# Performance work log

Hardware: AMD Instinct MI355X
Metric: run time of the kernel (lower is better)

Reference implementation:

```python
import jax, jax.numpy as jnp
import numpy as np
from jax import lax

B, T, C = 8, 1025, 512
HEADS = 8
CACHE = 256          # int(dim * cache_ratio)
CLS = 1
L = 256              # gr_cache memory length
H = W = 32           # sqrt(T - CLS)
EPS = 1e-5


def setup_inputs() -> dict:
    key = jax.random.key(0)
    ks = jax.random.split(key, 40)
    def w(k, shape, scale=0.02):
        return jax.random.normal(k, shape, dtype=jnp.float32) * scale
    inp = {}
    inp['x'] = jax.random.normal(ks[0], (B, T, C), dtype=jnp.float32)
    inp['gr_cache'] = jax.random.normal(ks[1], (1, L, CACHE), dtype=jnp.float32)
    # self-attention (dim=512) params, weights stored (in, out)
    inp['Wq1'] = w(ks[2], (C, C)); inp['bq1'] = jnp.zeros((C,), jnp.float32)
    inp['Wk1'] = w(ks[3], (C, C)); inp['bk1'] = jnp.zeros((C,), jnp.float32)
    inp['Wv1'] = w(ks[4], (C, C)); inp['bv1'] = jnp.zeros((C,), jnp.float32)
    inp['Wo1'] = w(ks[5], (C, C)); inp['bo1'] = jnp.zeros((C,), jnp.float32)
    # memory attention (dim=cache_dim=256) params
    inp['Wq2'] = w(ks[6], (CACHE, CACHE)); inp['bq2'] = jnp.zeros((CACHE,), jnp.float32)
    inp['Wk2'] = w(ks[7], (CACHE, CACHE)); inp['bk2'] = jnp.zeros((CACHE,), jnp.float32)
    inp['Wv2'] = w(ks[8], (CACHE, CACHE)); inp['bv2'] = jnp.zeros((CACHE,), jnp.float32)
    inp['Wo2'] = w(ks[9], (CACHE, CACHE)); inp['bo2'] = jnp.zeros((CACHE,), jnp.float32)
    # GRU-style gate linears: in = 2*cache_dim, out = cache_dim
    inp['Wr'] = w(ks[10], (2 * CACHE, CACHE)); inp['br'] = jnp.zeros((CACHE,), jnp.float32)
    inp['Wz'] = w(ks[11], (2 * CACHE, CACHE)); inp['bz'] = jnp.zeros((CACHE,), jnp.float32)
    inp['Wa'] = w(ks[12], (2 * CACHE, CACHE)); inp['ba'] = jnp.zeros((CACHE,), jnp.float32)
    # LayerNorm(cache_dim)
    inp['gamma'] = jnp.ones((CACHE,), jnp.float32)
    inp['beta'] = jnp.zeros((CACHE,), jnp.float32)
    # per-head gate logits, init to -1 as in the module
    inp['lam'] = jnp.full((HEADS,), -1.0, dtype=jnp.float32)
    # grouped conv pos-emb: Conv2d(512, 512, k=3, groups=CACHE) -> (O=512, I/g=2, 3, 3)
    inp['conv_w'] = w(ks[13], (C, C // CACHE, 3, 3))
    inp['conv_b'] = jnp.zeros((C,), jnp.float32)
    return inp


def _mha(q_in, kv_in, Wq, bq, Wk, bk, Wv, bv, Wo, bo):
    Bq, Tq, D = q_in.shape
    Tk = kv_in.shape[1]
    dh = D // HEADS
    q = (q_in @ Wq + bq).reshape(Bq, Tq, HEADS, dh)
    k = (kv_in @ Wk + bk).reshape(Bq, Tk, HEADS, dh)
    v = (kv_in @ Wv + bv).reshape(Bq, Tk, HEADS, dh)
    s = jnp.einsum('bqhd,bkhd->bhqk', q, k) * (1.0 / np.sqrt(dh)).astype(np.float32)
    a = jax.nn.softmax(s, axis=-1)
    o = jnp.einsum('bhqk,bkhd->bqhd', a, v).reshape(Bq, Tq, D)
    return o @ Wo + bo


def reference(x, gr_cache, Wq1, bq1, Wk1, bk1, Wv1, bv1, Wo1, bo1,
              Wq2, bq2, Wk2, bk2, Wv2, bv2, Wo2, bo2,
              Wr, br, Wz, bz, Wa, ba, gamma, beta, lam, conv_w, conv_b):
    B_, T_, C_ = x.shape
    # ---- spatial positional embedding (faithful to torch view->permute quirk) ----
    tok = x[:, CLS:, :].reshape(B_, H, W, C_).transpose(0, 3, 1, 2)   # (B, C, H, W)
    pos = lax.conv_general_dilated(tok, conv_w, (1, 1), 'SAME',
                                   feature_group_count=CACHE,
                                   dimension_numbers=('NCHW', 'OIHW', 'NCHW'))
    pos = pos + conv_b[None, :, None, None]
    pos = pos.reshape(B_, C_, T_ - CLS).transpose(0, 2, 1)            # (B, T-1, C)
    pos = jnp.concatenate([jnp.zeros((B_, CLS, C_), pos.dtype), pos], axis=1)
    # ---- self attention ----
    x_self = _mha(x, x, Wq1, bq1, Wk1, bk1, Wv1, bv1, Wo1, bo1)       # (B, T, C)
    x_self_h = x_self.reshape(B_, T_, HEADS, C_ // HEADS)
    # ---- GRU-style gated cache update ----
    gr = jnp.broadcast_to(gr_cache, (B_, L, CACHE))
    x_summary = x_self[:, :, :CACHE]
    idx = (jnp.arange(L) * T_) // L                                   # nearest interpolate T -> L
    x_summary = x_summary[:, idx, :]                                  # (B, L, CACHE)
    cat = jnp.concatenate([gr, x_summary], axis=-1)
    reset = jax.nn.sigmoid(cat @ Wr + br)
    z = jax.nn.sigmoid(cat @ Wz + bz)
    cat2 = jnp.concatenate([reset * gr, x_summary], axis=-1)
    add = jax.nn.gelu(cat2 @ Wa + ba, approximate=False)
    mu = add.mean(-1, keepdims=True)
    var = ((add - mu) ** 2).mean(-1, keepdims=True)
    add = (add - mu) / jnp.sqrt(var + EPS) * gamma + beta             # LayerNorm
    gr_new = z * add + (1.0 - z) * gr
    # ---- memory attention on first cache_dim channels ----
    x_mem = _mha(x[:, :, :CACHE], gr_new, Wq2, bq2, Wk2, bk2, Wv2, bv2, Wo2, bo2)
    x_mem = x_mem.reshape(B_, T_, HEADS, CACHE // HEADS)
    # ---- per-head alpha blend with zero-padded mem branch ----
    alpha = jax.nn.sigmoid(lam).reshape(1, 1, HEADS, 1)
    pad = jnp.zeros((B_, T_, HEADS, (C_ - CACHE) // HEADS), x.dtype)
    out = (alpha * jnp.concatenate([x_mem, pad], axis=-1)
           + (1.0 - alpha) * x_self_h).reshape(B_, T_, C_) + pos
    return out
```

## Files before the change

kernel.cpp:

```cpp
#include <hip/hip_runtime.h>
#include <math.h>

typedef unsigned short u16;
typedef unsigned int u32;
typedef __attribute__((ext_vector_type(8))) short short8;
typedef __attribute__((ext_vector_type(4))) short short4v;
typedef __attribute__((ext_vector_type(4))) float f32x4;

constexpr int Bc = 8;
constexpr int Tt = 1025;
constexpr int Cc = 512;
constexpr int Hn = 8;
constexpr int CA = 256;
constexpr int Ll = 256;

#if __has_builtin(__builtin_amdgcn_exp2f)
#define EXP2F __builtin_amdgcn_exp2f
#else
#define EXP2F exp2f
#endif

__device__ __forceinline__ u16 f2bf(float f) {
  u32 u = __builtin_bit_cast(u32, f);
  u = (u + 0x7FFFu + ((u >> 16) & 1u)) >> 16;
  return (u16)u;
}
__device__ __forceinline__ u32 pack2f(float lo, float hi) {
  const u32 a = __builtin_bit_cast(u32, hi) + 0x8000u;
  const u32 b = __builtin_bit_cast(u32, lo) + 0x8000u;
  return __builtin_amdgcn_perm(a, b, 0x07060302u);
}

struct WC { const float* s; u16* d; int sN; int sK; int kshift; int tot; };
struct WCP { WC w[11]; };

__global__ void wcast_k(WCP p) {
  const WC a = p.w[blockIdx.y];
  const int kmask = (1 << a.kshift) - 1;
  for (int idx = blockIdx.x * 256 + threadIdx.x; idx < a.tot; idx += gridDim.x * 256) {
    const int k = idx & kmask;
    const int n = idx >> a.kshift;
    a.d[idx] = (k < a.sK) ? f2bf(a.s[(size_t)k * a.sN + n]) : (u16)0;
  }
}

enum { EP_NONE = 0, EP_SIGMOID = 1, EP_GELU = 2 };

struct GemmEpi {
  const float* bias[4];
  int start[4];
  float scale[4];
  int nreg;
};

template <int AF32, int OUTBF, int ACT>
__global__ __launch_bounds__(256) void gemm_mfma(
    const void* __restrict__ Av, int lda,
    const u16* __restrict__ Wt,
    GemmEpi epi,
    void* __restrict__ Cout,
    int M, int N, int K)
{
  __shared__ u16 As[128][32];
  __shared__ u16 Bs[128][32];
  const int tid = threadIdx.x;
  const int m0 = blockIdx.y * 128, n0 = blockIdx.x * 128;
  const int ln = tid & 15, quad = (tid >> 4) & 3, wv = tid >> 6;
  const int wm = (wv & 1) * 64, wn = (wv >> 1) * 64;
  const int sr = tid >> 1;
  const int sk = (tid & 1) * 16;

  f32x4 zf = {0.f, 0.f, 0.f, 0.f};
  f32x4 acc[4][4];
  #pragma unroll
  for (int i = 0; i < 4; i++)
    #pragma unroll
    for (int j = 0; j < 4; j++) acc[i][j] = zf;

  const short8 z8 = {0, 0, 0, 0, 0, 0, 0, 0};

  for (int k0 = 0; k0 < K; k0 += 32) {
    const int gm = m0 + sr;
    short8 a0 = z8, a1 = z8;
    if (gm < M) {
      if (AF32) {
        const float* p = (const float*)Av + (size_t)gm * lda + k0 + sk;
        const float4 f0 = *(const float4*)(p + 0);
        const float4 f1 = *(const float4*)(p + 4);
        const float4 f2 = *(const float4*)(p + 8);
        const float4 f3 = *(const float4*)(p + 12);
        ((u32*)&a0)[0] = pack2f(f0.x, f0.y);
        ((u32*)&a0)[1] = pack2f(f0.z, f0.w);
        ((u32*)&a0)[2] = pack2f(f1.x, f1.y);
        ((u32*)&a0)[3] = pack2f(f1.z, f1.w);
        ((u32*)&a1)[0] = pack2f(f2.x, f2.y);
        ((u32*)&a1)[1] = pack2f(f2.z, f2.w);
        ((u32*)&a1)[2] = pack2f(f3.x, f3.y);
        ((u32*)&a1)[3] = pack2f(f3.z, f3.w);
      } else {
        const u16* p = (const u16*)Av + (size_t)gm * lda + k0 + sk;
        a0 = *(const short8*)p;
        a1 = *(const short8*)(p + 8);
      }
    }
    *(short8*)&As[sr][sk] = a0;
    *(short8*)&As[sr][sk + 8] = a1;
    {
      const u16* q = Wt + (size_t)(n0 + sr) * K + k0 + sk;
      *(short8*)&Bs[sr][sk] = *(const short8*)q;
      *(short8*)&Bs[sr][sk + 8] = *(const short8*)(q + 8);
    }
    __syncthreads();

    short8 af[4], bf[4];
    #pragma unroll
    for (int i = 0; i < 4; i++) af[i] = *(const short8*)&As[wm + i * 16 + ln][quad * 8];
    #pragma unroll
    for (int j = 0; j < 4; j++) bf[j] = *(const short8*)&Bs[wn + j * 16 + ln][quad * 8];
    #pragma unroll
    for (int i = 0; i < 4; i++)
      #pragma unroll
      for (int j = 0; j < 4; j++)
        acc[i][j] = __builtin_amdgcn_mfma_f32_16x16x32_bf16(af[i], bf[j], acc[i][j], 0, 0, 0);
    __syncthreads();
  }

  int ri = 0;
  #pragma unroll
  for (int i = 1; i < 4; i++)
    if (i < epi.nreg && epi.start[i] <= n0) ri = i;
  const float* bp = epi.bias[ri] - epi.start[ri];
  const float sc = epi.scale[ri];

  float bj[4];
  #pragma unroll
  for (int j = 0; j < 4; j++) bj[j] = bp[n0 + wn + j * 16 + ln];

  #pragma unroll
  for (int i = 0; i < 4; i++) {
    #pragma unroll
    for (int r = 0; r < 4; r++) {
      const int gm = m0 + wm + i * 16 + quad * 4 + r;
      if (gm >= M) continue;
      #pragma unroll
      for (int j = 0; j < 4; j++) {
        float v = (acc[i][j][r] + bj[j]) * sc;
        if (ACT == EP_SIGMOID)   v = 1.f / (1.f + __expf(-v));
        else if (ACT == EP_GELU) v = 0.5f * v * (1.f + erff(v * 0.70710678118654752f));
        const size_t off = (size_t)gm * N + n0 + wn + j * 16 + ln;
        if (OUTBF) ((u16*)Cout)[off] = f2bf(v);
        else       ((float*)Cout)[off] = v;
      }
    }
  }
}

template <int DH>
__global__ __launch_bounds__(256) void attn_mfma(
    const u16* __restrict__ Qp, const u16* __restrict__ Kp,
    const u16* __restrict__ Vp, u16* __restrict__ Op,
    int Tq, int Tk, int qbs, int kbs, int obs, int qrs, int krs, int ors)
{
  constexpr int NC = DH / 32;
  constexpr int NM = DH / 16;
  constexpr int VTE = 2 * DH * 32;
  constexpr int PAY = 2 * NM * 4 + 2;
  constexpr int PSTR = PAY | 1;

  __shared__ __align__(16) char smem[2 * VTE * 2 + 4 * 1024 * 2];
  static_assert(128 * PSTR * 4 <= 2 * VTE * 2 + 4 * 1024 * 2, "combine fits");
  u16* const VtP = (u16*)smem;
  u16* const PbP = (u16*)(smem + 2 * VTE * 2);

  const int b = blockIdx.y >> 3, h = blockIdx.y & 7;
  const int q0 = blockIdx.x * 64;
  const int tid = threadIdx.x;
  const int wv = tid >> 6;
  const int pair = wv >> 1;
  const int wvp = wv & 1;
  const int lane = tid & 63;
  const int ln = lane & 15, quad = lane >> 4;
  const int lt = tid & 127;

  const u16* Qb = Qp + (size_t)b * qbs + h * DH;
  const u16* Kb = Kp + (size_t)b * kbs + h * DH;
  const u16* Vb = Vp + (size_t)b * kbs + h * DH;
  u16* Ob = Op + (size_t)b * obs + h * DH;

  const short8 z8 = {0, 0, 0, 0, 0, 0, 0, 0};
  const f32x4 zf = {0.f, 0.f, 0.f, 0.f};

  short8 qf[2][NC];
  #pragma unroll
  for (int qs = 0; qs < 2; qs++) {
    const int gq = q0 + wvp * 32 + qs * 16 + ln;
    #pragma unroll
    for (int c = 0; c < NC; c++) {
      if (gq < Tq) qf[qs][c] = *(const short8*)(Qb + (size_t)gq * qrs + c * 32 + quad * 8);
      else         qf[qs][c] = z8;
    }
  }

  f32x4 oacc[2][NM];
  float lsum[2] = {0.f, 0.f};
  #pragma unroll
  for (int qs = 0; qs < 2; qs++)
    #pragma unroll
    for (int c = 0; c < NM; c++) oacc[qs][c] = zf;

  const int vd0 = (lt & 15) * (DH / 16);
  const int vk = (lt >> 4) * 4;
  const int gb = vk >> 3, off = vk & 7;

  const int nfull = Tk >> 5;
  const int nit = (Tk + 31) >> 5;
  const int tkm1 = Tk - 1;
  const int np = (nit + 1) >> 1;
  const int it0 = pair * np;
  const int itE = it0 + np;

  auto loadK = [&](int it, short8 (&kf)[2][NC]) {
    #pragma unroll
    for (int kc = 0; kc < 2; kc++)
      #pragma unroll
      for (int c = 0; c < NC; c++) {
        int row = (it << 5) + kc * 16 + ln;
        row = row < tkm1 ? row : tkm1;
        kf[kc][c] = *(const short8*)(Kb + (size_t)row * krs + c * 32 + quad * 8);
      }
  };
  auto loadV = [&](int it, short4v (&vr)[4]) {
    #pragma unroll
    for (int i2 = 0; i2 < 4; i2++) {
      int gk = (it << 5) + vk + i2;
      gk = gk < tkm1 ? gk : tkm1;
      short4v t = {0, 0, 0, 0};
      if (DH == 64) {
        t = *(const short4v*)(Vb + (size_t)gk * krs + vd0);
      } else {
        ushort2 u = *(const ushort2*)(Vb + (size_t)gk * krs + vd0);
        t[0] = (short)u.x; t[1] = (short)u.y;
      }
      vr[i2] = t;
    }
  };

  auto body = [&](int it, short8 (&kfC)[2][NC], short4v (&vrC)[4],
                  short8 (&kfN)[2][NC], short4v (&vrN)[4]) {
    const bool full = (it < nfull);
    u16* vt = VtP + pair * VTE + (it & 1) * (DH * 32);
    const int k0 = it << 5;

    #pragma unroll
    for (int i = 0; i < DH / 16; i++) {
      const int d = vd0 + i;
      const int h2 = (d ^ (d >> 3)) & 3;
      short4v w = {vrC[0][i], vrC[1][i], vrC[2][i], vrC[3][i]};
      *(short4v*)&vt[d * 32 + ((gb ^ h2) << 3) + off] = w;
    }
    if (it + 1 < itE) { loadK(it + 1, kfN); loadV(it + 1, vrN); }
    __syncthreads();

    #pragma unroll
    for (int qs = 0; qs < 2; qs++) {
      #pragma unroll
      for (int kc = 0; kc < 2; kc++) {
        f32x4 s = zf;
        #pragma unroll
        for (int c = 0; c < NC; c++)
          s = __builtin_amdgcn_mfma_f32_16x16x32_bf16(kfC[kc][c], qf[qs][c], s, 0, 0, 0);
        float p0, p1, p2, p3;
        if (full) {
          p0 = EXP2F(s[0]); p1 = EXP2F(s[1]); p2 = EXP2F(s[2]); p3 = EXP2F(s[3]);
        } else {
          const int kb = k0 + kc * 16 + quad * 4;
          p0 = (kb + 0 < Tk) ? EXP2F(s[0]) : 0.f;
          p1 = (kb + 1 < Tk) ? EXP2F(s[1]) : 0.f;
          p2 = (kb + 2 < Tk) ? EXP2F(s[2]) : 0.f;
          p3 = (kb + 3 < Tk) ? EXP2F(s[3]) : 0.f;
        }
        lsum[qs] += (p0 + p1) + (p2 + p3);
        short4v pw;
        ((u32*)&pw)[0] = pack2f(p0, p1);
        ((u32*)&pw)[1] = pack2f(p2, p3);
        const int q = qs * 16 + ln;
        const int g = ((kc * 2 + (quad >> 1)) ^ (ln & 3)) & 3;
        *(short4v*)&PbP[wv * 1024 + q * 32 + (g << 3) + (quad & 1) * 4] = pw;
      }
    }

    short8 pf2[2];
    #pragma unroll
    for (int qs = 0; qs < 2; qs++) {
      const int q = qs * 16 + ln;
      const int g = quad ^ (ln & 3);
      pf2[qs] = *(const short8*)&PbP[wv * 1024 + q * 32 + g * 8];
    }
    #pragma unroll
    for (int c = 0; c < NM; c++) {
      const int d = c * 16 + ln;
      const int g = quad ^ ((d ^ (d >> 3)) & 3);
      const short8 vf = *(const short8*)&vt[d * 32 + g * 8];
      #pragma unroll
      for (int qs = 0; qs < 2; qs++)
        oacc[qs][c] = __builtin_amdgcn_mfma_f32_16x16x32_bf16(pf2[qs], vf, oacc[qs][c], 0, 0, 0);
    }
  };

  short8 kfA[2][NC], kfB[2][NC];
  short4v vrA[4], vrB[4];
  loadK(it0, kfA);
  loadV(it0, vrA);

  int j = 0;
  for (; j + 1 < np; j += 2) {
    body(it0 + j, kfA, vrA, kfB, vrB);
    body(it0 + j + 1, kfB, vrB, kfA, vrA);
  }
  if (j < np) body(it0 + j, kfA, vrA, kfB, vrB);

  __syncthreads();
  float* const cbuf = (float*)smem;
  if (wv >= 2) {
    float* dst = cbuf + ((wv - 2) * 64 + lane) * PSTR;
    int idx = 0;
    #pragma unroll
    for (int qs = 0; qs < 2; qs++)
      #pragma unroll
      for (int c = 0; c < NM; c++)
        #pragma unroll
        for (int r = 0; r < 4; r++) dst[idx++] = oacc[qs][c][r];
    dst[idx++] = lsum[0];
    dst[idx]   = lsum[1];
  }
  __syncthreads();
  if (wv >= 2) return;
  {
    const float* src = cbuf + (wv * 64 + lane) * PSTR;
    int idx = 0;
    #pragma unroll
    for (int qs = 0; qs < 2; qs++)
      #pragma unroll
      for (int c = 0; c < NM; c++)
        #pragma unroll
        for (int r = 0; r < 4; r++) oacc[qs][c][r] += src[idx++];
    lsum[0] += src[idx++];
    lsum[1] += src[idx];
  }

  float lq[2];
  #pragma unroll
  for (int qs = 0; qs < 2; qs++) {
    float t = lsum[qs];
    t += __shfl_xor(t, 16);
    t += __shfl_xor(t, 32);
    lq[qs] = t;
  }
  #pragma unroll
  for (int qs = 0; qs < 2; qs++) {
    #pragma unroll
    for (int r = 0; r < 4; r++) {
      const float linv = 1.f / __shfl(lq[qs], quad * 4 + r);
      const int gq = q0 + wvp * 32 + qs * 16 + quad * 4 + r;
      if (gq >= Tq) continue;
      #pragma unroll
      for (int c = 0; c < NM; c++)
        Ob[(size_t)gq * ors + c * 16 + ln] = f2bf(oacc[qs][c][r] * linv);
    }
  }
}

__global__ __launch_bounds__(256) void conv_combine(
    const float* __restrict__ x, const float* __restrict__ cw,
    const float* __restrict__ cb, const float* __restrict__ x_self,
    const float* __restrict__ x_mem, const float* __restrict__ lam,
    float* __restrict__ out)
{
  const int bh = blockIdx.x;
  const int b = bh >> 5, hh = bh & 31;
  const int c = (blockIdx.y << 8) + threadIdx.x;
  const int ci = c & ~1;
  const int dd = c & 63;
  const int h8 = c >> 6;
  const float alpha = 1.f / (1.f + __expf(-lam[h8]));
  const float bias = cb[c];

  float wgt[2][9];
  #pragma unroll
  for (int ch = 0; ch < 2; ch++)
    #pragma unroll
    for (int k = 0; k < 9; k++) wgt[ch][k] = cw[c * 18 + ch * 9 + k];

  const float* xrow[3];
  bool rv[3];
  #pragma unroll
  for (int r = 0; r < 3; r++) {
    const int h2 = hh + r - 1;
    rv[r] = (unsigned)h2 < 32u;
    xrow[r] = x + ((size_t)(b * Tt) + 1 + h2 * 32) * Cc + ci;
  }

  float2 win[3][3];
  #pragma unroll
  for (int r = 0; r < 3; r++) {
    win[r][0] = make_float2(0.f, 0.f);
    win[r][1] = rv[r] ? *(const float2*)(xrow[r]) : make_float2(0.f, 0.f);
  }

  const size_t bT = (size_t)b * Tt;
  for (int w = 0; w < 32; w++) {
    #pragma unroll
    for (int r = 0; r < 3; r++)
      win[r][2] = (rv[r] && w + 1 < 32) ? *(const float2*)(xrow[r] + (w + 1) * Cc)
                                        : make_float2(0.f, 0.f);
    float pos = bias;
    #pragma unroll
    for (int r = 0; r < 3; r++)
      #pragma unroll
      for (int col = 0; col < 3; col++) {
        pos += win[r][col].x * wgt[0][r * 3 + col];
        pos += win[r][col].y * wgt[1][r * 3 + col];
      }
    const size_t bt = bT + 1 + hh * 32 + w;
    const float mem = (dd < 32) ? x_mem[bt * 256 + h8 * 32 + dd] : 0.f;
    out[bt * 512 + c] = pos + alpha * mem + (1.f - alpha) * x_self[bt * 512 + c];
    #pragma unroll
    for (int r = 0; r < 3; r++) { win[r][0] = win[r][1]; win[r][1] = win[r][2]; }
  }

  if (hh == 0) {
    const float mem = (dd < 32) ? x_mem[bT * 256 + h8 * 32 + dd] : 0.f;
    out[bT * 512 + c] = alpha * mem + (1.f - alpha) * x_self[bT * 512 + c];
  }
}

__global__ void build_cat(const float* __restrict__ gr_cache,
                          const float* __restrict__ x_self,
                          u16* __restrict__ cat)
{
  const int idx = blockIdx.x * 256 + threadIdx.x;
  if (idx >= Bc * Ll * 512) return;
  const int k = idx & 511;
  const int bi = idx >> 9;
  const int i = bi & 255;
  const int b = bi >> 8;
  float v;
  if (k < 256) v = gr_cache[i * 256 + k];
  else         v = x_self[((size_t)(b * Tt + 4 * i)) * Cc + (k - 256)];
  cat[idx] = f2bf(v);
}

__global__ void build_cat2(const float* __restrict__ gr_cache,
                           const float* __restrict__ rzg,
                           u16* __restrict__ cat)
{
  const int idx = blockIdx.x * 256 + threadIdx.x;
  if (idx >= Bc * Ll * 256) return;
  const int k = idx & 255;
  const int bi = idx >> 8;
  const int i = bi & 255;
  cat[(size_t)bi * 512 + k] = f2bf(gr_cache[i * 256 + k] * rzg[(size_t)bi * 512 + k]);
}

__device__ inline float block_sum256(float v, float* red)
{
  #pragma unroll
  for (int o = 32; o >= 1; o >>= 1) v += __shfl_down(v, o);
  const int wid = threadIdx.x >> 6;
  if ((threadIdx.x & 63) == 0) red[wid] = v;
  __syncthreads();
  const float t = red[0] + red[1] + red[2] + red[3];
  __syncthreads();
  return t;
}

__global__ __launch_bounds__(256) void ln_gate(
    const float* __restrict__ add_raw, const float* __restrict__ rzg,
    const float* __restrict__ gr_cache, const float* __restrict__ gamma,
    const float* __restrict__ beta, u16* __restrict__ gr_new)
{
  __shared__ float red[4];
  const int bi = blockIdx.x;
  const int i = bi & 255;
  const int c = threadIdx.x;
  const float v = add_raw[(size_t)bi * 256 + c];
  const float mu = block_sum256(v, red) * (1.f / 256.f);
  const float dv = v - mu;
  const float var = block_sum256(dv * dv, red) * (1.f / 256.f);
  const float nrm = dv * rsqrtf(var + 1e-5f) * gamma[c] + beta[c];
  const float zz = rzg[(size_t)bi * 512 + 256 + c];
  gr_new[(size_t)bi * 256 + c] = f2bf(zz * nrm + (1.f - zz) * gr_cache[i * 256 + c]);
}

extern "C" void kernel_launch(void* const* d_in, const int* in_sizes, int n_in,
                              void* d_out, int out_size, void* d_ws, size_t ws_size,
                              hipStream_t stream)
{
  const float* x        = (const float*)d_in[0];
  const float* gr_cache = (const float*)d_in[1];
  const float* Wq1 = (const float*)d_in[2];  const float* bq1 = (const float*)d_in[3];
  const float* Wk1 = (const float*)d_in[4];  const float* bk1 = (const float*)d_in[5];
  const float* Wv1 = (const float*)d_in[6];  const float* bv1 = (const float*)d_in[7];
  const float* Wo1 = (const float*)d_in[8];  const float* bo1 = (const float*)d_in[9];
  const float* Wq2 = (const float*)d_in[10]; const float* bq2 = (const float*)d_in[11];
  const float* Wk2 = (const float*)d_in[12]; const float* bk2 = (const float*)d_in[13];
  const float* Wv2 = (const float*)d_in[14]; const float* bv2 = (const float*)d_in[15];
  const float* Wo2 = (const float*)d_in[16]; const float* bo2 = (const float*)d_in[17];
  const float* Wr  = (const float*)d_in[18]; const float* br  = (const float*)d_in[19];
  const float* Wz  = (const float*)d_in[20]; const float* bz  = (const float*)d_in[21];
  const float* Wa  = (const float*)d_in[22]; const float* ba  = (const float*)d_in[23];
  const float* gamma = (const float*)d_in[24];
  const float* beta  = (const float*)d_in[25];
  const float* lam   = (const float*)d_in[26];
  const float* conv_w = (const float*)d_in[27];
  const float* conv_b = (const float*)d_in[28];
  float* out = (float*)d_out;

  const int M1 = Bc * Tt;
  const int M2 = Bc * Ll;
  const size_t BLA = (size_t)Bc * Ll * CA;
  const size_t BL2 = (size_t)Bc * Ll * 512;

  char* W = (char*)d_ws;
  u16*   qkvq  = (u16*)(W + 0);
  u16*   att1  = (u16*)(W + 29388800);
  u16*   att2  = (u16*)(W + 29388800);
  float* x_self= (float*)(W + 37785600);
  u16*   cat   = (u16*)(W + 54579200);
  float* rzg   = (float*)(W + 56676352);
  float* addr_ = (float*)(W + 60870656);
  float* x_mem = (float*)(W + 54579200);
  u16*   gr_new= (u16*)(W + 62976000);
  u16*   k2v2  = (u16*)(W + 64024576);
  u16*   wtb   = (u16*)(W + 66121728);

  u16* megaW = wtb;
  u16* o1W   = wtb + 917504;
  u16* rzW   = wtb + 1179648;
  u16* aW    = wtb + 1441792;
  u16* kvW   = wtb + 1572864;
  u16* o2W   = wtb + 1703936;

  const dim3 blk(256);

  {
    WCP p;
    p.w[0]  = {Wq1, megaW + 0,           512, 512, 9, 512 * 512};
    p.w[1]  = {Wk1, megaW + 512 * 512,   512, 512, 9, 512 * 512};
    p.w[2]  = {Wv1, megaW + 1024 * 512,  512, 512, 9, 512 * 512};
    p.w[3]  = {Wq2, megaW + 1536 * 512,  256, 256, 9, 256 * 512};
    p.w[4]  = {Wo1, o1W,                 512, 512, 9, 512 * 512};
    p.w[5]  = {Wr,  rzW + 0,             256, 512, 9, 256 * 512};
    p.w[6]  = {Wz,  rzW + 256 * 512,     256, 512, 9, 256 * 512};
    p.w[7]  = {Wa,  aW,                  256, 512, 9, 256 * 512};
    p.w[8]  = {Wk2, kvW + 0,             256, 256, 8, 256 * 256};
    p.w[9]  = {Wv2, kvW + 256 * 256,     256, 256, 8, 256 * 256};
    p.w[10] = {Wo2, o2W,                 256, 256, 8, 256 * 256};
    wcast_k<<<dim3(64, 11), blk, 0, stream>>>(p);
  }

  const float sQ1 = 0.18033688011112042f;
  const float sQ2 = 0.25503490664918414f;

  {
    GemmEpi e;
    e.bias[0] = bq1; e.start[0] = 0;    e.scale[0] = sQ1;
    e.bias[1] = bk1; e.start[1] = 512;  e.scale[1] = 1.f;
    e.bias[2] = bv1; e.start[2] = 1024; e.scale[2] = 1.f;
    e.bias[3] = bq2; e.start[3] = 1536; e.scale[3] = sQ2;
    e.nreg = 4;
    gemm_mfma<1, 1, EP_NONE><<<dim3(14, 65), blk, 0, stream>>>(
        x, 512, megaW, e, qkvq, M1, 1792, 512);
  }

  attn_mfma<64><<<dim3(17, 64), dim3(256), 0, stream>>>(
      qkvq, qkvq + 512, qkvq + 1024, att1, Tt, Tt,
      Tt * 1792, Tt * 1792, Tt * 512, 1792, 1792, 512);

  {
    GemmEpi e; e.bias[0] = bo1; e.start[0] = 0; e.scale[0] = 1.f; e.nreg = 1;
    gemm_mfma<0, 0, EP_NONE><<<dim3(4, 65), blk, 0, stream>>>(
        att1, 512, o1W, e, x_self, M1, 512, 512);
  }

  build_cat<<<(int)((BL2 + 255) / 256), blk, 0, stream>>>(gr_cache, x_self, cat);
  {
    GemmEpi e;
    e.bias[0] = br; e.start[0] = 0;   e.scale[0] = 1.f;
    e.bias[1] = bz; e.start[1] = 256; e.scale[1] = 1.f;
    e.nreg = 2;
    gemm_mfma<0, 0, EP_SIGMOID><<<dim3(4, 16), blk, 0, stream>>>(
        cat, 512, rzW, e, rzg, M2, 512, 512);
  }
  build_cat2<<<(int)((BLA + 255) / 256), blk, 0, stream>>>(gr_cache, rzg, cat);
  {
    GemmEpi e; e.bias[0] = ba; e.start[0] = 0; e.scale[0] = 1.f; e.nreg = 1;
    gemm_mfma<0, 0, EP_GELU><<<dim3(2, 16), blk, 0, stream>>>(
        cat, 512, aW, e, addr_, M2, 256, 512);
  }
  ln_gate<<<M2, blk, 0, stream>>>(addr_, rzg, gr_cache, gamma, beta, gr_new);

  {
    GemmEpi e;
    e.bias[0] = bk2; e.start[0] = 0;   e.scale[0] = 1.f;
    e.bias[1] = bv2; e.start[1] = 256; e.scale[1] = 1.f;
    e.nreg = 2;
    gemm_mfma<0, 1, EP_NONE><<<dim3(4, 16), blk, 0, stream>>>(
        gr_new, 256, kvW, e, k2v2, M2, 512, 256);
  }

  attn_mfma<32><<<dim3(17, 64), dim3(256), 0, stream>>>(
      qkvq + 1536, k2v2, k2v2 + 256, att2, Tt, Ll,
      Tt * 1792, Ll * 512, Tt * 256, 1792, 512, 256);

  {
    GemmEpi e; e.bias[0] = bo2; e.start[0] = 0; e.scale[0] = 1.f; e.nreg = 1;
    gemm_mfma<0, 0, EP_NONE><<<dim3(2, 65), blk, 0, stream>>>(
        att2, 256, o2W, e, x_mem, M1, 256, 256);
  }

  conv_combine<<<dim3(Bc * 32, 2), blk, 0, stream>>>(x, conv_w, conv_b, x_self,
                                                     x_mem, lam, out);
}
```

Measured before the change: 359.6 us.

## Process two key tiles per barrier with four-slot V staging in attention

The attention loop now stages two V tiles into shared memory before each barrier, using four LDS slots per wave pair, which halves the number of __syncthreads calls. Prefetch of the next two K/V tiles is interleaved with the score and PV MFMA work so global loads overlap compute. The cost is double the V staging LDS, more live prefetch registers, and a possible occupancy drop.

```diff
diff --git a/kernel.cpp b/kernel.cpp
--- a/kernel.cpp
+++ b/kernel.cpp
@@ -163,14 +163,14 @@
 {
   constexpr int NC = DH / 32;
   constexpr int NM = DH / 16;
-  constexpr int VTE = 2 * DH * 32;
+  constexpr int VT1 = DH * 32;
   constexpr int PAY = 2 * NM * 4 + 2;
   constexpr int PSTR = PAY | 1;
 
-  __shared__ __align__(16) char smem[2 * VTE * 2 + 4 * 1024 * 2];
-  static_assert(128 * PSTR * 4 <= 2 * VTE * 2 + 4 * 1024 * 2, "combine fits");
+  __shared__ __align__(16) char smem[2 * 4 * VT1 * 2 + 4 * 1024 * 2];
+  static_assert(128 * PSTR * 4 <= 2 * 4 * VT1 * 2 + 4 * 1024 * 2, "combine fits");
   u16* const VtP = (u16*)smem;
-  u16* const PbP = (u16*)(smem + 2 * VTE * 2);
+  u16* const PbP = (u16*)(smem + 2 * 4 * VT1 * 2);
 
   const int b = blockIdx.y >> 3, h = blockIdx.y & 7;
   const int q0 = blockIdx.x * 64;
@@ -218,6 +218,8 @@
   const int np = (nit + 1) >> 1;
   const int it0 = pair * np;
   const int itE = it0 + np;
+
+  u16* const pvb = VtP + pair * (4 * VT1);
 
   auto loadK = [&](int it, short8 (&kf)[2][NC]) {
     #pragma unroll
@@ -245,12 +247,7 @@
     }
   };
 
-  auto body = [&](int it, short8 (&kfC)[2][NC], short4v (&vrC)[4],
-                  short8 (&kfN)[2][NC], short4v (&vrN)[4]) {
-    const bool full = (it < nfull);
-    u16* vt = VtP + pair * VTE + (it & 1) * (DH * 32);
-    const int k0 = it << 5;
-
+  auto stageV = [&](const short4v (&vrC)[4], u16* vt) {
     #pragma unroll
     for (int i = 0; i < DH / 16; i++) {
       const int d = vd0 + i;
@@ -258,9 +255,11 @@
       short4v w = {vrC[0][i], vrC[1][i], vrC[2][i], vrC[3][i]};
       *(short4v*)&vt[d * 32 + ((gb ^ h2) << 3) + off] = w;
     }
-    if (it + 1 < itE) { loadK(it + 1, kfN); loadV(it + 1, vrN); }
-    __syncthreads();
-
+  };
+
+  auto scoreP = [&](int it, const short8 (&kfC)[2][NC]) {
+    const bool full = (it < nfull);
+    const int k0 = it << 5;
     #pragma unroll
     for (int qs = 0; qs < 2; qs++) {
       #pragma unroll
@@ -288,7 +287,9 @@
         *(short4v*)&PbP[wv * 1024 + q * 32 + (g << 3) + (quad & 1) * 4] = pw;
       }
     }
-
+  };
+
+  auto pv = [&](const u16* vt) {
     short8 pf2[2];
     #pragma unroll
     for (int qs = 0; qs < 2; qs++) {
@@ -309,15 +310,35 @@
 
   short8 kfA[2][NC], kfB[2][NC];
   short4v vrA[4], vrB[4];
+  loadV(it0, vrA);
   loadK(it0, kfA);
-  loadV(it0, vrA);
-
-  int j = 0;
-  for (; j + 1 < np; j += 2) {
-    body(it0 + j, kfA, vrA, kfB, vrB);
-    body(it0 + j + 1, kfB, vrB, kfA, vrA);
-  }
-  if (j < np) body(it0 + j, kfA, vrA, kfB, vrB);
+  if (it0 + 1 < itE) { loadV(it0 + 1, vrB); loadK(it0 + 1, kfB); }
+
+  int j = it0;
+  for (; j + 1 < itE; j += 2) {
+    const int ph = ((j - it0) >> 1) & 1;
+    u16* vt0 = pvb + (ph * 2 + 0) * VT1;
+    u16* vt1 = pvb + (ph * 2 + 1) * VT1;
+    stageV(vrA, vt0);
+    stageV(vrB, vt1);
+    __syncthreads();
+    if (j + 2 < itE) loadV(j + 2, vrA);
+    if (j + 3 < itE) loadV(j + 3, vrB);
+    scoreP(j, kfA);
+    if (j + 2 < itE) loadK(j + 2, kfA);
+    pv(vt0);
+    scoreP(j + 1, kfB);
+    if (j + 3 < itE) loadK(j + 3, kfB);
+    pv(vt1);
+  }
+  if (j < itE) {
+    const int ph = ((j - it0) >> 1) & 1;
+    u16* vt0 = pvb + (ph * 2 + 0) * VT1;
+    stageV(vrA, vt0);
+    __syncthreads();
+    scoreP(j, kfA);
+    pv(vt0);
+  }
 
   __syncthreads();
   float* const cbuf = (float*)smem;
```

Measured after the change: 386.8 us. +7.6%, slower.
